# Performance work log

Measured on AMD Instinct MI355X. Metric: run time of the kernel, lower is better.

## Reference

```python
import jax, jax.numpy as jnp
import numpy as np

D_MODEL = 1024
D_INNER = 2048
D_STATE = 16
D_CONV = 4
DT_RANK = 64  # ceil(D_MODEL / 16)
BATCH = 2
SEQLEN = 2048


def setup_inputs() -> dict:
    key = jax.random.key(0)
    ks = jax.random.split(key, 9)
    s = 0.02
    hidden_states = jax.random.normal(ks[0], (BATCH, SEQLEN, D_MODEL), dtype=jnp.float32)
    W_in = jax.random.normal(ks[1], (D_MODEL, 2 * D_INNER), dtype=jnp.float32) * s
    # flax depthwise Conv kernel layout: (window, in_features//groups=1, out_features)
    conv_kernel = jax.random.normal(ks[2], (D_CONV, 1, D_INNER), dtype=jnp.float32) * 0.2
    conv_bias = jax.random.normal(ks[3], (D_INNER,), dtype=jnp.float32) * s
    W_x = jax.random.normal(ks[4], (D_INNER, DT_RANK + 2 * D_STATE), dtype=jnp.float32) * s
    W_dt = jax.random.normal(ks[5], (DT_RANK, D_INNER), dtype=jnp.float32) * s
    b_dt = jax.random.normal(ks[6], (D_INNER,), dtype=jnp.float32) * s
    # A_log = log(arange(1, d_state+1)) broadcast over d_inner (constant init in module)
    A_log = jnp.log(jnp.broadcast_to(jnp.arange(1, D_STATE + 1, dtype=jnp.float32), (D_INNER, D_STATE)))
    D = jnp.ones((D_INNER,), dtype=jnp.float32)
    W_out = jax.random.normal(ks[7], (D_INNER, D_MODEL), dtype=jnp.float32) * s
    return {
        "hidden_states": hidden_states,
        "W_in": W_in,
        "conv_kernel": conv_kernel,
        "conv_bias": conv_bias,
        "W_x": W_x,
        "W_dt": W_dt,
        "b_dt": b_dt,
        "A_log": A_log,
        "D": D,
        "W_out": W_out,
    }


def _mamba_forward(hidden_states, W_in, conv_kernel, conv_bias, W_x, W_dt, b_dt, A_log, D, W_out):
    # in_proj, then einops '(d i)' split with i=2 => interleaved channels
    xz = hidden_states @ W_in                       # (b, l, 2*d_inner)
    x = xz[..., 0::2]                               # (b, l, d_inner)
    z = xz[..., 1::2]                               # (b, l, d_inner)

    # depthwise conv1d, padding='SAME' (as in flax nn.Conv)
    x = jax.lax.conv_general_dilated(
        x, conv_kernel, window_strides=(1,), padding="SAME",
        dimension_numbers=("NWC", "WIO", "NWC"),
        feature_group_count=D_INNER,
    ) + conv_bias
    x = jax.nn.silu(x)

    x_dbl = x @ W_x                                 # (b, l, dt_rank + 2*d_state)
    dt = x_dbl[..., :DT_RANK] @ W_dt + b_dt         # (b, l, d_inner)
    Bm = x_dbl[..., DT_RANK:DT_RANK + D_STATE]      # (b, l, n)
    Cm = x_dbl[..., DT_RANK + D_STATE:]             # (b, l, n)

    A = -jnp.exp(A_log.astype(jnp.float32))         # (d_inner, n)
    delta = jax.nn.softplus(dt.astype(jnp.float32)) # (b, l, d_inner)

    deltaA = jnp.exp(jnp.einsum("bld,dn->lbdn", delta, A))          # (l, b, d, n)
    deltaB_u = jnp.einsum("bld,bln,bld->lbdn", delta, Bm, x)        # (l, b, d, n)
    C_l = jnp.transpose(Cm, (1, 0, 2))                               # (l, b, n)

    state0 = jnp.zeros((BATCH, D_INNER, D_STATE), dtype=jnp.float32)

    def step(state, inputs):
        dA, dBu, c = inputs
        state = dA * state + dBu                    # (b, d, n)
        y = jnp.einsum("bdn,bn->bd", state, c)      # (b, d)
        return state, y

    _, y = jax.lax.scan(step, state0, (deltaA, deltaB_u, C_l))
    y = jnp.transpose(y, (1, 0, 2))                 # (b, l, d_inner)

    out = (y + x * D) * jax.nn.silu(z)              # skip via D, gate via silu(z)
    return out @ W_out                              # (b, l, d_model)


def reference(hidden_states, W_in, conv_kernel, conv_bias, W_x, W_dt, b_dt, A_log, D, W_out):
    return _mamba_forward(hidden_states, W_in, conv_kernel, conv_bias, W_x, W_dt, b_dt, A_log, D, W_out)
```

## Files before the change

### kernel.cpp

```cpp
#include <hip/hip_runtime.h>
#include <hip/hip_bf16.h>

typedef unsigned short u16;
typedef __attribute__((ext_vector_type(8))) short short8;
typedef __attribute__((ext_vector_type(4))) short short4v;
typedef __attribute__((ext_vector_type(4))) float f32x4;
typedef __attribute__((ext_vector_type(4))) float float4v;
typedef __attribute__((ext_vector_type(2))) float f32x2;

#define DMODEL 1024
#define DI 2048
#define NST 16
#define RANK 64
#define BB 2
#define LL 2048
#define MM (BB*LL)
#define LC 32
#define NCH (LL/LC)

__device__ __forceinline__ float b2f(u16 v){ union{unsigned u; float f;}x; x.u=(unsigned)v<<16; return x.f; }
__device__ __forceinline__ u16 f2b(float f){
  union{unsigned u; float f;}x; x.f=f;
  unsigned r = x.u + 0x7FFFu + ((x.u>>16)&1u);
  return (u16)(r>>16);
}
__device__ __forceinline__ bool probe_bf(const u16* probe){ return probe[1] != 0; }
__device__ __forceinline__ float ldin(const void* p, size_t i, bool bf){
  return bf ? b2f(((const u16*)p)[i]) : ((const float*)p)[i];
}
__device__ __forceinline__ u16 ldb(const void* p, size_t i, bool bf){
  return bf ? ((const u16*)p)[i] : f2b(((const float*)p)[i]);
}
__device__ __forceinline__ void gl16(const u16* g, char* lds_wave_base){
  __builtin_amdgcn_global_load_lds((const __attribute__((address_space(1))) unsigned*)g,
                                   (__attribute__((address_space(3))) unsigned*)lds_wave_base, 16, 0, 0);
}

template<int EPI>
__global__ __launch_bounds__(256,2) void mgemm_k(
    const u16* __restrict__ A, const u16* __restrict__ Bt,
    void* __restrict__ O0, void* __restrict__ O1,
    const void* __restrict__ bias, const u16* __restrict__ probe,
    int M, int N, int K, int lda, int ldb, int ldc)
{
  const bool bf = probe_bf(probe);
  __shared__ char smem[(EPI==3) ? 33792 : 16384];
  const int t = threadIdx.x;
  const int m0 = blockIdx.y*128, n0 = blockIdx.x*128;
  const int kbeg = blockIdx.z * K;
  const int lane = t & 63;
  const int wv = t >> 6;
  const int wm = (wv>>1)*64, wn = (wv&1)*64;
  const int lr = lane & 15, q = lane >> 4;

  const int r0 = t>>2, q0 = t&3;
  const u16* Ag0 = A + kbeg + (size_t)(m0 + r0)*lda + q0*8;
  const u16* Ag1 = A + kbeg + (size_t)(m0 + 64 + r0)*lda + q0*8;
  const u16* Bg0 = Bt + kbeg + (size_t)(n0 + r0)*ldb + q0*8;
  const u16* Bg1 = Bt + kbeg + (size_t)(n0 + 64 + r0)*ldb + q0*8;
  char* const wbase = smem + (t & ~63)*16;
  char* const lA0 = wbase;
  char* const lA1 = wbase + 4096;
  char* const lB0 = wbase + 8192;
  char* const lB1 = wbase + 12288;

  int aro[4], bro[4];
#pragma unroll
  for(int i=0;i<4;i++) aro[i] = (wm + i*16 + lr)*64 + q*16;
#pragma unroll
  for(int j=0;j<4;j++) bro[j] = (wn + j*16 + lr)*64 + q*16;

  f32x4 acc[4][4];
#pragma unroll
  for(int i=0;i<4;i++)
#pragma unroll
    for(int j=0;j<4;j++) acc[i][j] = (f32x4){0.f,0.f,0.f,0.f};

  for(int k0=0;k0<K;k0+=32){
    __syncthreads();
    gl16(Ag0 + k0, lA0); gl16(Ag1 + k0, lA1);
    gl16(Bg0 + k0, lB0); gl16(Bg1 + k0, lB1);
    __syncthreads();
    short8 af[4], bfv[4];
#pragma unroll
    for(int i=0;i<4;i++) af[i] = *(const short8*)(smem + aro[i]);
#pragma unroll
    for(int j=0;j<4;j++) bfv[j] = *(const short8*)(smem + 8192 + bro[j]);
#pragma unroll
    for(int i=0;i<4;i++)
#pragma unroll
      for(int j=0;j<4;j++)
        acc[i][j] = __builtin_amdgcn_mfma_f32_16x16x32_bf16(af[i], bfv[j], acc[i][j], 0,0,0);
  }

  if(EPI==3){
    float bj[4];
#pragma unroll
    for(int j=0;j<4;j++) bj[j] = ldin(bias, n0 + wn + j*16 + lr, bf);
    __syncthreads();
    u16* tile = (u16*)smem;
#pragma unroll
    for(int i=0;i<4;i++)
#pragma unroll
      for(int r=0;r<4;r++){
        int trow = wm + i*16 + q*4 + r;
#pragma unroll
        for(int j=0;j<4;j++){
          int tcol = wn + j*16 + lr;
          float s = acc[i][j][r] + bj[j];
          float sp = (s > 20.f) ? s : log1pf(__expf(s));
          tile[trow*132 + tcol] = f2b(sp);
        }
      }
    __syncthreads();
#pragma unroll
    for(int it=0;it<8;it++){
      int idx = it*256 + t;
      int row = idx >> 4;
      int colc = (idx & 15) * 8;
      short8 v = *(const short8*)(tile + row*132 + colc);
      *(short8*)((u16*)O0 + (size_t)(m0+row)*ldc + n0 + colc) = v;
    }
    return;
  }
#pragma unroll
  for(int i=0;i<4;i++){
#pragma unroll
    for(int r=0;r<4;r++){
      int row = m0 + wm + i*16 + q*4 + r;
#pragma unroll
      for(int j=0;j<4;j++){
        int col = n0 + wn + j*16 + lr;
        float v = acc[i][j][r];
        if(EPI==0){
          if(col & 1) ((u16*)O1)[(size_t)row*DI + (col>>1)] = f2b(v);
          else        ((u16*)O0)[(size_t)row*DI + (col>>1)] = f2b(v);
        } else if(EPI==1){
          ((float*)O0)[(size_t)blockIdx.z*M*ldc + (size_t)row*ldc + col] = v;
        } else {
          if(bf) ((u16*)O0)[(size_t)row*ldc + col] = f2b(v);
          else   ((float*)O0)[(size_t)row*ldc + col] = v;
        }
      }
    }
  }
}

__device__ __forceinline__ void tr_block(
    const void* src, u16* dst, int R, int C, int bx, int by, bool bf, int tid, u16 (*tile)[33])
{
  const int c0 = bx*32, r0 = by*32;
  const int tc = tid & 31, tr0 = tid >> 5;
#pragma unroll
  for(int i=0;i<4;i++){
    int r = tr0 + i*8;
    int gc = c0 + tc;
    tile[r][tc] = (gc < C) ? ldb(src, (size_t)(r0+r)*C + gc, bf) : (u16)0;
  }
  __syncthreads();
#pragma unroll
  for(int i=0;i<4;i++){
    int dr = c0 + tr0 + i*8;
    int dc = r0 + tc;
    dst[(size_t)dr*R + dc] = tile[tc][tr0 + i*8];
  }
}

__global__ __launch_bounds__(256) void prep_k(
    const void* __restrict__ W_in, const void* __restrict__ W_out,
    const void* __restrict__ W_x, const void* __restrict__ W_dt,
    const void* __restrict__ hidden,
    u16* __restrict__ WinT, u16* __restrict__ WoutT, u16* __restrict__ WxT,
    u16* __restrict__ WdtT, u16* __restrict__ hb, const u16* __restrict__ probe)
{
  const bool bf = probe_bf(probe);
  __shared__ u16 tile[32][33];
  const int bid = blockIdx.x, t = threadIdx.x;
  if(bid < 4096){
    tr_block(W_in, WinT, DMODEL, 2*DI, bid & 127, bid >> 7, bf, t, tile);
  } else if(bid < 6144){
    int b2 = bid - 4096; tr_block(W_out, WoutT, DI, DMODEL, b2 & 31, b2 >> 5, bf, t, tile);
  } else if(bid < 6400){
    int b2 = bid - 6144; tr_block(W_x, WxT, DI, 96, b2 & 3, b2 >> 2, bf, t, tile);
  } else if(bid < 6528){
    int b2 = bid - 6400; tr_block(W_dt, WdtT, RANK, DI, b2 & 63, b2 >> 6, bf, t, tile);
  } else {
    size_t i = ((size_t)(bid - 6528)*256 + t)*8;
    if(bf){
      *(short8*)(hb+i) = *(const short8*)((const u16*)hidden + i);
    } else {
      float4v a = *(const float4v*)((const float*)hidden + i);
      float4v b = *(const float4v*)((const float*)hidden + i + 4);
      short8 r;
      r[0]=(short)f2b(a[0]); r[1]=(short)f2b(a[1]); r[2]=(short)f2b(a[2]); r[3]=(short)f2b(a[3]);
      r[4]=(short)f2b(b[0]); r[5]=(short)f2b(b[1]); r[6]=(short)f2b(b[2]); r[7]=(short)f2b(b[3]);
      *(short8*)(hb+i) = r;
    }
  }
}

__global__ __launch_bounds__(256) void redx_k(
    const float* __restrict__ P, float* __restrict__ xdbl, u16* __restrict__ xdblb)
{
  size_t i = ((size_t)blockIdx.x*256 + threadIdx.x)*4;
  float4v a = *(const float4v*)(P + i);
  float4v b = *(const float4v*)(P + (size_t)MM*128 + i);
  float4v s = a + b;
  *(float4v*)(xdbl + i) = s;
  short4v r; r[0]=(short)f2b(s[0]); r[1]=(short)f2b(s[1]); r[2]=(short)f2b(s[2]); r[3]=(short)f2b(s[3]);
  *(short4v*)(xdblb + i) = r;
}

__global__ __launch_bounds__(256) void red7_k(
    const float* __restrict__ P, void* __restrict__ out, const u16* __restrict__ probe)
{
  const bool bf = probe_bf(probe);
  size_t i = ((size_t)blockIdx.x*256 + threadIdx.x)*4;
  float4v a = *(const float4v*)(P + i);
  float4v b = *(const float4v*)(P + (size_t)MM*DMODEL + i);
  float4v s = a + b;
  if(bf){
    short4v r; r[0]=(short)f2b(s[0]); r[1]=(short)f2b(s[1]); r[2]=(short)f2b(s[2]); r[3]=(short)f2b(s[3]);
    *(short4v*)((u16*)out + i) = r;
  } else {
    *(float4v*)((float*)out + i) = s;
  }
}

__global__ __launch_bounds__(256) void conv_silu_k(
  const u16* __restrict__ xb, const void* __restrict__ w,
  const void* __restrict__ bias, u16* __restrict__ xcb,
  const u16* __restrict__ probe)
{
  const bool bf = probe_bf(probe);
  const int row = blockIdx.x;
  const int tt = row & (LL-1);
  const int d = threadIdx.x*8;
  float wv[4][8], bv[8];
  if(bf){
    short8 bb = *(const short8*)((const u16*)bias + d);
#pragma unroll
    for(int j=0;j<8;j++) bv[j] = b2f((u16)bb[j]);
#pragma unroll
    for(int k=0;k<4;k++){
      short8 ww = *(const short8*)((const u16*)w + k*DI + d);
#pragma unroll
      for(int j=0;j<8;j++) wv[k][j] = b2f((u16)ww[j]);
    }
  } else {
    *(float4v*)(bv)   = *(const float4v*)((const float*)bias + d);
    *(float4v*)(bv+4) = *(const float4v*)((const float*)bias + d + 4);
#pragma unroll
    for(int k=0;k<4;k++){
      *(float4v*)(wv[k])   = *(const float4v*)((const float*)w + k*DI + d);
      *(float4v*)(wv[k]+4) = *(const float4v*)((const float*)w + k*DI + d + 4);
    }
  }
  float acc[8];
#pragma unroll
  for(int j=0;j<8;j++) acc[j] = bv[j];
  const u16* xrow = xb + (size_t)row*DI + d;
#pragma unroll
  for(int k=0;k<4;k++){
    int o = tt - 1 + k;
    if(0<=o && o<LL){
      short8 xv = *(const short8*)(xrow + (ptrdiff_t)(k-1)*DI);
#pragma unroll
      for(int j=0;j<8;j++) acc[j] = fmaf(b2f((u16)xv[j]), wv[k][j], acc[j]);
    }
  }
  short8 sb;
#pragma unroll
  for(int j=0;j<8;j++){ float s = acc[j] / (1.f + __expf(-acc[j])); sb[j]=(short)f2b(s); }
  *(short8*)(xcb + (size_t)row*DI + d) = sb;
}

__global__ __launch_bounds__(256) void scan_a_k(
  const u16* __restrict__ dlb, const u16* __restrict__ xcb,
  const float* __restrict__ xdbl, const void* __restrict__ A_log,
  float* __restrict__ Bacc, float* __restrict__ sumdv,
  const u16* __restrict__ probe)
{
  const bool bf = probe_bf(probe);
  __shared__ float Bsh[LC][NST];
  const int t = threadIdx.x;
  const int d0 = blockIdx.x*512 + 2*t;
  const int b = blockIdx.y, c = blockIdx.z;
  for(int i=t;i<LC*NST;i+=256){
    int l = i>>4, n = i&15;
    Bsh[l][n] = xdbl[((size_t)b*LL + (size_t)c*LC + l)*128 + 64 + n];
  }
  __syncthreads();
  float ac[2][NST], s[2][NST];
#pragma unroll
  for(int ch=0;ch<2;ch++)
#pragma unroll
    for(int n=0;n<NST;n++){
      ac[ch][n] = -__expf(ldin(A_log, (size_t)(d0+ch)*NST+n, bf));
      s[ch][n]=0.f;
    }
  bool geom = true;
#pragma unroll
  for(int ch=0;ch<2;ch++){
    float a0 = ac[ch][0];
#pragma unroll
    for(int n=1;n<NST;n++) geom = geom && (fabsf(ac[ch][n]-(n+1)*a0) <= 1e-4f*(n+1)*fabsf(a0));
  }
  float sum0=0.f, sum1=0.f;
  const size_t base0 = ((size_t)b*LL + (size_t)c*LC)*DI + d0;
  for(int l=0;l<LC;l++){
    unsigned dp = *(const unsigned*)(dlb + base0 + (size_t)l*DI);
    unsigned xp = *(const unsigned*)(xcb + base0 + (size_t)l*DI);
    float dv0=b2f((u16)(dp&0xffff)), dv1=b2f((u16)(dp>>16));
    float xv0=b2f((u16)(xp&0xffff)), xv1=b2f((u16)(xp>>16));
    float du0=dv0*xv0, du1=dv1*xv1;
    sum0+=dv0; sum1+=dv1;
    if(geom){
      float e0=__expf(ac[0][0]*dv0), e1=__expf(ac[1][0]*dv1);
      float p0=1.f, p1=1.f;
#pragma unroll
      for(int n=0;n<NST;n++){
        float Bv=Bsh[l][n];
        p0*=e0; s[0][n]=fmaf(p0, s[0][n], du0*Bv);
        p1*=e1; s[1][n]=fmaf(p1, s[1][n], du1*Bv);
      }
    } else {
#pragma unroll
      for(int n=0;n<NST;n++){
        float Bv=Bsh[l][n];
        s[0][n]=fmaf(__expf(ac[0][n]*dv0), s[0][n], du0*Bv);
        s[1][n]=fmaf(__expf(ac[1][n]*dv1), s[1][n], du1*Bv);
      }
    }
  }
  const size_t ob = ((size_t)c*BB + b)*((size_t)NST*DI) + d0;
#pragma unroll
  for(int n=0;n<NST;n++){
    f32x2 bs; bs[0]=s[0][n]; bs[1]=s[1][n];
    *(f32x2*)(Bacc + ob + (size_t)n*DI) = bs;
  }
  f32x2 sd; sd[0]=sum0; sd[1]=sum1;
  *(f32x2*)(sumdv + ((size_t)c*BB + b)*DI + d0) = sd;
}

__global__ __launch_bounds__(256) void scan_b_k(
  const float* __restrict__ Bacc, const float* __restrict__ sumdv,
  const void* __restrict__ A_log, float* __restrict__ Sin,
  const u16* __restrict__ probe)
{
  const bool bf = probe_bf(probe);
  const int idx = blockIdx.x*256 + threadIdx.x;
  const int d = idx & (DI-1);
  const int n = (idx >> 11) & 15;
  const int b = idx >> 15;
  const float ac = -__expf(ldin(A_log, (size_t)d*NST+n, bf));
  float s = 0.f;
  for(int c=0;c<NCH;c++){
    size_t off = (size_t)c*((size_t)BB*NST*DI) + idx;
    float a = __expf(ac * sumdv[((size_t)c*BB + b)*DI + d]);
    float bb = Bacc[off];
    Sin[off] = s;
    s = fmaf(a, s, bb);
  }
}

__global__ __launch_bounds__(256) void scan_c_gate_k(
  const u16* __restrict__ dlb, const u16* __restrict__ xcb,
  const float* __restrict__ xdbl, const void* __restrict__ A_log,
  const float* __restrict__ Sin, const u16* __restrict__ zb,
  const void* __restrict__ Dw, u16* __restrict__ G,
  const u16* __restrict__ probe)
{
  const bool bf = probe_bf(probe);
  __shared__ float Bsh[LC][NST], Csh[LC][NST];
  const int t = threadIdx.x;
  const int d0 = blockIdx.x*512 + 2*t;
  const int b = blockIdx.y, c = blockIdx.z;
  for(int i=t;i<LC*NST;i+=256){
    int l = i>>4, n = i&15;
    size_t ro = ((size_t)b*LL + (size_t)c*LC + l)*128;
    Bsh[l][n] = xdbl[ro + 64 + n];
    Csh[l][n] = xdbl[ro + 80 + n];
  }
  __syncthreads();
  float ac[2][NST], s[2][NST];
  const size_t ib = ((size_t)c*BB + b)*((size_t)NST*DI) + d0;
#pragma unroll
  for(int ch=0;ch<2;ch++)
#pragma unroll
    for(int n=0;n<NST;n++)
      ac[ch][n] = -__expf(ldin(A_log, (size_t)(d0+ch)*NST+n, bf));
#pragma unroll
  for(int n=0;n<NST;n++){
    f32x2 si = *(const f32x2*)(Sin + ib + (size_t)n*DI);
    s[0][n]=si[0]; s[1][n]=si[1];
  }
  bool geom = true;
#pragma unroll
  for(int ch=0;ch<2;ch++){
    float a0 = ac[ch][0];
#pragma unroll
    for(int n=1;n<NST;n++) geom = geom && (fabsf(ac[ch][n]-(n+1)*a0) <= 1e-4f*(n+1)*fabsf(a0));
  }
  const float D0 = ldin(Dw, d0, bf), D1 = ldin(Dw, d0+1, bf);
  const size_t base0 = ((size_t)b*LL + (size_t)c*LC)*DI + d0;
  for(int l=0;l<LC;l++){
    const size_t idx = base0 + (size_t)l*DI;
    unsigned dp = *(const unsigned*)(dlb + idx);
    unsigned xp = *(const unsigned*)(xcb + idx);
    unsigned zz = *(const unsigned*)(zb + idx);
    float dv0=b2f((u16)(dp&0xffff)), dv1=b2f((u16)(dp>>16));
    float xv0=b2f((u16)(xp&0xffff)), xv1=b2f((u16)(xp>>16));
    float du0=dv0*xv0, du1=dv1*xv1;
    float y0=0.f, y1=0.f;
    if(geom){
      float e0=__expf(ac[0][0]*dv0), e1=__expf(ac[1][0]*dv1);
      float p0=1.f, p1=1.f;
#pragma unroll
      for(int n=0;n<NST;n++){
        float Bv=Bsh[l][n], Cv=Csh[l][n];
        p0*=e0; s[0][n]=fmaf(p0, s[0][n], du0*Bv); y0=fmaf(s[0][n], Cv, y0);
        p1*=e1; s[1][n]=fmaf(p1, s[1][n], du1*Bv); y1=fmaf(s[1][n], Cv, y1);
      }
    } else {
#pragma unroll
      for(int n=0;n<NST;n++){
        float Bv=Bsh[l][n], Cv=Csh[l][n];
        s[0][n]=fmaf(__expf(ac[0][n]*dv0), s[0][n], du0*Bv); y0=fmaf(s[0][n], Cv, y0);
        s[1][n]=fmaf(__expf(ac[1][n]*dv1), s[1][n], du1*Bv); y1=fmaf(s[1][n], Cv, y1);
      }
    }
    float z0 = b2f((u16)(zz & 0xffff)), z1 = b2f((u16)(zz >> 16));
    float g0 = z0 / (1.f + __expf(-z0));
    float g1 = z1 / (1.f + __expf(-z1));
    float o0 = (y0 + xv0*D0) * g0;
    float o1 = (y1 + xv1*D1) * g1;
    *(unsigned*)(G + idx) = (unsigned)f2b(o0) | ((unsigned)f2b(o1) << 16);
  }
}

extern "C" void kernel_launch(void* const* d_in, const int* in_sizes, int n_in,
                              void* d_out, int out_size, void* d_ws, size_t ws_size,
                              hipStream_t stream)
{
  const void* hidden = d_in[0];
  const void* W_in   = d_in[1];
  const void* convw  = d_in[2];
  const void* convb  = d_in[3];
  const void* W_x    = d_in[4];
  const void* W_dt   = d_in[5];
  const void* b_dt   = d_in[6];
  const u16*  A_log  = (const u16*)d_in[7];
  const void* Dw     = d_in[8];
  const void* W_out  = d_in[9];

  char* p = (char*)d_ws;
  u16*   xb   = (u16*)  p;
  float* Sin  = (float*)p;
  u16*   zb   = (u16*)  (p + 16777216);
  u16*   xcb  = (u16*)  (p + 33554432);
  float* Bcc  = (float*)(p + 67108864);
  u16*   G    = (u16*)  (p + 83886080);
  float* Pw   = (float*)(p + 100663296);
  u16*   dlb  = (u16*)  (p + 100663296);
  float* Pw7  = (float*)(p + 100663296);
  u16*   hb   = (u16*)  (p + 117440512);
  float* sumdv= (float*)(p + 117440512);
  float* xdbl = (float*)(p + 134217728);
  u16*   xdblb= (u16*)  (p + 136314880);
  u16*   WinT = (u16*)  (p + 137363456);
  u16*   WoutT= (u16*)  (p + 145752064);
  u16*   WxT  = (u16*)  (p + 149946368);
  u16*   WdtT = (u16*)  (p + 150470656);

  prep_k<<<6528 + (MM*DMODEL)/(256*8), 256, 0, stream>>>(
      W_in, W_out, W_x, W_dt, hidden, WinT, WoutT, WxT, WdtT, hb, A_log);
  mgemm_k<0><<<dim3(32,32), 256, 0, stream>>>(hb, WinT, xb, zb, nullptr, A_log,
                                              MM, 2*DI, DMODEL, DMODEL, DMODEL, 0);
  conv_silu_k<<<MM, 256, 0, stream>>>(xb, convw, convb, xcb, A_log);
  mgemm_k<1><<<dim3(1,32,2), 256, 0, stream>>>(xcb, WxT, Pw, nullptr, nullptr, A_log,
                                               MM, 128, DI/2, DI, DI, 128);
  redx_k<<<(MM*128)/(256*4), 256, 0, stream>>>(Pw, xdbl, xdblb);
  mgemm_k<3><<<dim3(16,32), 256, 0, stream>>>(xdblb, WdtT, dlb, nullptr, b_dt, A_log,
                                              MM, DI, RANK, 128, RANK, DI);
  scan_a_k<<<dim3(DI/512, BB, NCH), 256, 0, stream>>>(dlb, xcb, xdbl, A_log, Bcc, sumdv, A_log);
  scan_b_k<<<(BB*NST*DI)/256, 256, 0, stream>>>(Bcc, sumdv, A_log, Sin, A_log);
  scan_c_gate_k<<<dim3(DI/512, BB, NCH), 256, 0, stream>>>(dlb, xcb, xdbl, A_log, Sin, zb, Dw, G, A_log);
  mgemm_k<1><<<dim3(DMODEL/128, MM/128, 2), 256, 0, stream>>>(G, WoutT, Pw7, nullptr, nullptr, A_log,
                                                              MM, DMODEL, DI/2, DI, DI, DMODEL);
  red7_k<<<(MM*DMODEL)/(256*4), 256, 0, stream>>>(Pw7, d_out, A_log);
}
```

Measured before the change: 343.6 us.

## Permute W_in columns for coalesced x/z epilogue, swizzle GEMM tiles, deepen split-K

The transposed W_in rows are permuted so x and z columns become contiguous halves. The in_proj GEMM can then write each tile through LDS with vectorised stores instead of scattered interleaved 2-byte stores. A workgroup index swizzle is added to all GEMMs to improve L2 reuse, and the x_proj GEMM's split-K grows from 2 to 8 to raise parallelism, with a matching wider reduction. The scan chunk length doubles from 32 to 64, which halves the number of chunks but lengthens each serial chunk.

```diff
diff --git a/kernel.cpp b/kernel.cpp
--- a/kernel.cpp
+++ b/kernel.cpp
@@ -15,7 +15,7 @@
 #define BB 2
 #define LL 2048
 #define MM (BB*LL)
-#define LC 32
+#define LC 64
 #define NCH (LL/LC)
 
 __device__ __forceinline__ float b2f(u16 v){ union{unsigned u; float f;}x; x.u=(unsigned)v<<16; return x.f; }
@@ -44,9 +44,17 @@
     int M, int N, int K, int lda, int ldb, int ldc)
 {
   const bool bf = probe_bf(probe);
-  __shared__ char smem[(EPI==3) ? 33792 : 16384];
+  __shared__ char smem[(EPI==3||EPI==4) ? 33792 : 16384];
   const int t = threadIdx.x;
-  const int m0 = blockIdx.y*128, n0 = blockIdx.x*128;
+  int bx = blockIdx.x, by = blockIdx.y;
+  {
+    const int gx = gridDim.x;
+    const int nwg = gx*gridDim.y;
+    const int lin = by*gx + bx;
+    const int swz = (lin & 7)*(nwg>>3) + (lin>>3);
+    bx = swz % gx; by = swz / gx;
+  }
+  const int m0 = by*128, n0 = bx*128;
   const int kbeg = blockIdx.z * K;
   const int lane = t & 63;
   const int wv = t >> 6;
@@ -93,10 +101,12 @@
         acc[i][j] = __builtin_amdgcn_mfma_f32_16x16x32_bf16(af[i], bfv[j], acc[i][j], 0,0,0);
   }
 
-  if(EPI==3){
+  if(EPI==3 || EPI==4){
     float bj[4];
-#pragma unroll
-    for(int j=0;j<4;j++) bj[j] = ldin(bias, n0 + wn + j*16 + lr, bf);
+    if(EPI==3){
+#pragma unroll
+      for(int j=0;j<4;j++) bj[j] = ldin(bias, n0 + wn + j*16 + lr, bf);
+    }
     __syncthreads();
     u16* tile = (u16*)smem;
 #pragma unroll
@@ -107,19 +117,27 @@
 #pragma unroll
         for(int j=0;j<4;j++){
           int tcol = wn + j*16 + lr;
-          float s = acc[i][j][r] + bj[j];
-          float sp = (s > 20.f) ? s : log1pf(__expf(s));
-          tile[trow*132 + tcol] = f2b(sp);
+          float v = acc[i][j][r];
+          if(EPI==3){
+            float s = v + bj[j];
+            v = (s > 20.f) ? s : log1pf(__expf(s));
+          }
+          tile[trow*132 + tcol] = f2b(v);
         }
       }
     __syncthreads();
+    u16* obase;
+    int cb;
+    if(EPI==4){ obase = (n0 < DI) ? (u16*)O0 : (u16*)O1; cb = n0 & (DI-1); }
+    else      { obase = (u16*)O0; cb = n0; }
+    const int oc = (EPI==4) ? DI : ldc;
 #pragma unroll
     for(int it=0;it<8;it++){
       int idx = it*256 + t;
       int row = idx >> 4;
       int colc = (idx & 15) * 8;
       short8 v = *(const short8*)(tile + row*132 + colc);
-      *(short8*)((u16*)O0 + (size_t)(m0+row)*ldc + n0 + colc) = v;
+      *(short8*)(obase + (size_t)(m0+row)*oc + cb + colc) = v;
     }
     return;
   }
@@ -132,10 +150,7 @@
       for(int j=0;j<4;j++){
         int col = n0 + wn + j*16 + lr;
         float v = acc[i][j][r];
-        if(EPI==0){
-          if(col & 1) ((u16*)O1)[(size_t)row*DI + (col>>1)] = f2b(v);
-          else        ((u16*)O0)[(size_t)row*DI + (col>>1)] = f2b(v);
-        } else if(EPI==1){
+        if(EPI==1){
           ((float*)O0)[(size_t)blockIdx.z*M*ldc + (size_t)row*ldc + col] = v;
         } else {
           if(bf) ((u16*)O0)[(size_t)row*ldc + col] = f2b(v);
@@ -147,7 +162,8 @@
 }
 
 __device__ __forceinline__ void tr_block(
-    const void* src, u16* dst, int R, int C, int bx, int by, bool bf, int tid, u16 (*tile)[33])
+    const void* src, u16* dst, int R, int C, int bx, int by, bool bf, bool perm,
+    int tid, u16 (*tile)[33])
 {
   const int c0 = bx*32, r0 = by*32;
   const int tc = tid & 31, tr0 = tid >> 5;
@@ -161,6 +177,7 @@
 #pragma unroll
   for(int i=0;i<4;i++){
     int dr = c0 + tr0 + i*8;
+    if(perm) dr = (dr>>1) + ((dr&1)<<11);
     int dc = r0 + tc;
     dst[(size_t)dr*R + dc] = tile[tc][tr0 + i*8];
   }
@@ -177,13 +194,13 @@
   __shared__ u16 tile[32][33];
   const int bid = blockIdx.x, t = threadIdx.x;
   if(bid < 4096){
-    tr_block(W_in, WinT, DMODEL, 2*DI, bid & 127, bid >> 7, bf, t, tile);
+    tr_block(W_in, WinT, DMODEL, 2*DI, bid & 127, bid >> 7, bf, true, t, tile);
   } else if(bid < 6144){
-    int b2 = bid - 4096; tr_block(W_out, WoutT, DI, DMODEL, b2 & 31, b2 >> 5, bf, t, tile);
+    int b2 = bid - 4096; tr_block(W_out, WoutT, DI, DMODEL, b2 & 31, b2 >> 5, bf, false, t, tile);
   } else if(bid < 6400){
-    int b2 = bid - 6144; tr_block(W_x, WxT, DI, 96, b2 & 3, b2 >> 2, bf, t, tile);
+    int b2 = bid - 6144; tr_block(W_x, WxT, DI, 96, b2 & 3, b2 >> 2, bf, false, t, tile);
   } else if(bid < 6528){
-    int b2 = bid - 6400; tr_block(W_dt, WdtT, RANK, DI, b2 & 63, b2 >> 6, bf, t, tile);
+    int b2 = bid - 6400; tr_block(W_dt, WdtT, RANK, DI, b2 & 63, b2 >> 6, bf, false, t, tile);
   } else {
     size_t i = ((size_t)(bid - 6528)*256 + t)*8;
     if(bf){
@@ -203,9 +220,9 @@
     const float* __restrict__ P, float* __restrict__ xdbl, u16* __restrict__ xdblb)
 {
   size_t i = ((size_t)blockIdx.x*256 + threadIdx.x)*4;
-  float4v a = *(const float4v*)(P + i);
-  float4v b = *(const float4v*)(P + (size_t)MM*128 + i);
-  float4v s = a + b;
+  float4v s = *(const float4v*)(P + i);
+#pragma unroll
+  for(int p=1;p<8;p++) s += *(const float4v*)(P + (size_t)p*MM*128 + i);
   *(float4v*)(xdbl + i) = s;
   short4v r; r[0]=(short)f2b(s[0]); r[1]=(short)f2b(s[1]); r[2]=(short)f2b(s[2]); r[3]=(short)f2b(s[3]);
   *(short4v*)(xdblb + i) = r;
@@ -475,11 +492,11 @@
 
   prep_k<<<6528 + (MM*DMODEL)/(256*8), 256, 0, stream>>>(
       W_in, W_out, W_x, W_dt, hidden, WinT, WoutT, WxT, WdtT, hb, A_log);
-  mgemm_k<0><<<dim3(32,32), 256, 0, stream>>>(hb, WinT, xb, zb, nullptr, A_log,
-                                              MM, 2*DI, DMODEL, DMODEL, DMODEL, 0);
+  mgemm_k<4><<<dim3(32,32), 256, 0, stream>>>(hb, WinT, xb, zb, nullptr, A_log,
+                                              MM, 2*DI, DMODEL, DMODEL, DMODEL, DI);
   conv_silu_k<<<MM, 256, 0, stream>>>(xb, convw, convb, xcb, A_log);
-  mgemm_k<1><<<dim3(1,32,2), 256, 0, stream>>>(xcb, WxT, Pw, nullptr, nullptr, A_log,
-                                               MM, 128, DI/2, DI, DI, 128);
+  mgemm_k<1><<<dim3(1,32,8), 256, 0, stream>>>(xcb, WxT, Pw, nullptr, nullptr, A_log,
+                                               MM, 128, DI/8, DI, DI, 128);
   redx_k<<<(MM*128)/(256*4), 256, 0, stream>>>(Pw, xdbl, xdblb);
   mgemm_k<3><<<dim3(16,32), 256, 0, stream>>>(xdblb, WdtT, dlb, nullptr, b_dt, A_log,
                                               MM, DI, RANK, 128, RANK, DI);
```

Measured after the change: 348.9 us. Within noise of the previous version (+1.5%).
